# Performance work log

Hardware: AMD Instinct MI355X
Metric: run time of the kernel (lower is better)

## Reference

```python
import jax, jax.numpy as jnp
import numpy as np

N_EXPERTS = 8
TOP_K = 2
D_MODEL = 1024
HIDDEN = 4096


def setup_inputs() -> dict:
    key = jax.random.key(0)
    ks = jax.random.split(key, 6)
    B, S = 4, 1024
    scale = 0.02
    x = jax.random.normal(ks[0], (B, S, D_MODEL), dtype=jnp.float32)
    # gate / noise linear weights, torch nn.Linear convention: (out, in)
    w_gate = jax.random.normal(ks[1], (N_EXPERTS, D_MODEL), dtype=jnp.float32) * scale
    w_noise = jax.random.normal(ks[2], (N_EXPERTS, D_MODEL), dtype=jnp.float32) * scale
    # stacked expert weights: w_g/w_u: (E, H, D), w_d: (E, D, H)
    w_g = jax.random.normal(ks[3], (N_EXPERTS, HIDDEN, D_MODEL), dtype=jnp.float32) * scale
    w_u = jax.random.normal(ks[4], (N_EXPERTS, HIDDEN, D_MODEL), dtype=jnp.float32) * scale
    w_d = jax.random.normal(ks[5], (N_EXPERTS, D_MODEL, HIDDEN), dtype=jnp.float32) * scale
    return {"x": x, "w_gate": w_gate, "w_noise": w_noise, "w_g": w_g, "w_u": w_u, "w_d": w_d}


def reference(x, w_gate, w_noise, w_g, w_u, w_d):
    B, S, D = x.shape
    T = B * S
    xf = x.reshape(T, D)

    # --- NoisyTopKGate (eval mode: no noise) ---
    logits = xf @ w_gate.T                                  # (T, E)
    top_logits, top_idx = jax.lax.top_k(logits, TOP_K)      # (T, K)
    top_gates = jax.nn.softmax(top_logits, axis=-1)         # (T, K)
    rows = jnp.arange(T)[:, None]
    gates = jnp.zeros_like(logits).at[rows, top_idx].set(top_gates)  # (T, E) sparse

    probs = jax.nn.softmax(logits, axis=-1)
    f = gates.mean(axis=0)
    P = probs.mean(axis=0)
    aux_loss = N_EXPERTS * jnp.sum(f * P)

    # --- expert loop (SwiGLU FFN); gate==0 zeroes non-routed contributions ---
    out = jnp.zeros_like(xf)
    for e in range(N_EXPERTS):
        hidden = jax.nn.silu(xf @ w_g[e].T) * (xf @ w_u[e].T)   # (T, H)
        y = hidden @ w_d[e].T                                    # (T, D)
        out = out + gates[:, e:e + 1] * y

    return out.reshape(B, S, D), aux_loss
```

## Files before the change

### kernel.cpp

```cpp
#include <hip/hip_runtime.h>

#define TT 4096
#define DM 1024
#define HH 4096
#define NE 8
#define NSLOT (TT*2)
#define TM 128
#define MAXTILES 72

typedef __bf16 bf16x8 __attribute__((ext_vector_type(8)));
typedef float f32x4 __attribute__((ext_vector_type(4)));

__device__ __forceinline__ unsigned short f2bs(float f) {
  unsigned u = __float_as_uint(f);
  u += 0x7fffu + ((u >> 16) & 1u);
  return (unsigned short)(u >> 16);
}
__device__ __forceinline__ float bs2f(unsigned short s) {
  return __uint_as_float(((unsigned)s) << 16);
}
__device__ __forceinline__ unsigned pk_rnd(float lo, float hi) {
  return ((__float_as_uint(lo) + 0x8000u) >> 16) |
         ((__float_as_uint(hi) + 0x8000u) & 0xffff0000u);
}
__device__ __forceinline__ void gld_lds16(const unsigned short* g, unsigned short* l) {
  __builtin_amdgcn_global_load_lds(
      (const __attribute__((address_space(1))) unsigned int*)g,
      (__attribute__((address_space(3))) unsigned int*)l, 16, 0, 0);
}

__global__ __launch_bounds__(256) void k_gate(
    const float* __restrict__ x, const float* __restrict__ w_gate,
    int* __restrict__ counts, float* __restrict__ gsum, float* __restrict__ psum,
    int* __restrict__ gidx, float* __restrict__ gval) {
  __shared__ float wg[NE * DM];
  __shared__ float bg[NE]; __shared__ float bp[NE]; __shared__ int bc[NE];
  int tid = threadIdx.x;
  for (int i = tid; i < NE * DM; i += 256) wg[i] = w_gate[i];
  if (tid < NE) { bg[tid] = 0.f; bp[tid] = 0.f; bc[tid] = 0; }
  __syncthreads();
  int wave = tid >> 6, lane = tid & 63;
  for (int it = 0; it < 4; ++it) {
    int t = blockIdx.x * 16 + wave * 4 + it;
    const float* xr = x + (size_t)t * DM;
    float s[NE];
#pragma unroll
    for (int e = 0; e < NE; ++e) s[e] = 0.f;
    for (int d = lane; d < DM; d += 64) {
      float xv = xr[d];
#pragma unroll
      for (int e = 0; e < NE; ++e) s[e] += xv * wg[e * DM + d];
    }
#pragma unroll
    for (int e = 0; e < NE; ++e) {
      float v = s[e];
      v += __shfl_down(v, 32); v += __shfl_down(v, 16); v += __shfl_down(v, 8);
      v += __shfl_down(v, 4);  v += __shfl_down(v, 2);  v += __shfl_down(v, 1);
      s[e] = v;
    }
    if (lane == 0) {
      int e1 = 0; float v1 = s[0];
      for (int e = 1; e < NE; ++e) if (s[e] > v1) { v1 = s[e]; e1 = e; }
      int e2 = -1; float v2 = -1e30f;
      for (int e = 0; e < NE; ++e) if (e != e1 && s[e] > v2) { v2 = s[e]; e2 = e; }
      float g1 = 1.f / (1.f + __expf(v2 - v1));
      float g2 = 1.f - g1;
      float psm = 0.f, p[NE];
      for (int e = 0; e < NE; ++e) { p[e] = __expf(s[e] - v1); psm += p[e]; }
      float inv = 1.f / psm;
      atomicAdd(&bg[e1], g1); atomicAdd(&bg[e2], g2);
      for (int e = 0; e < NE; ++e) atomicAdd(&bp[e], p[e] * inv);
      atomicAdd(&bc[e1], 1); atomicAdd(&bc[e2], 1);
      gidx[t * 2] = e1; gidx[t * 2 + 1] = e2;
      gval[t * 2] = g1; gval[t * 2 + 1] = g2;
    }
  }
  __syncthreads();
  if (tid < NE) {
    atomicAdd(&counts[tid], bc[tid]);
    atomicAdd(&gsum[tid], bg[tid]);
    atomicAdd(&psum[tid], bp[tid]);
  }
}

__global__ void k_plan(const int* __restrict__ counts, const float* __restrict__ gsum,
                       const float* __restrict__ psum, int* __restrict__ bases,
                       int* __restrict__ ntiles, int* __restrict__ tile_e,
                       int* __restrict__ tile_s0, int* __restrict__ tile_n,
                       float* __restrict__ aux_out) {
  if (threadIdx.x != 0 || blockIdx.x != 0) return;
  int base = 0, nt = 0;
  for (int e = 0; e < NE; ++e) {
    bases[e] = base;
    int c = counts[e];
    for (int s = 0; s < c; s += TM) {
      tile_e[nt] = e; tile_s0[nt] = base + s;
      tile_n[nt] = (c - s < TM) ? (c - s) : TM; ++nt;
    }
    base += c;
  }
  *ntiles = nt;
  float aux = 0.f;
  for (int e = 0; e < NE; ++e)
    aux += (gsum[e] / (float)TT) * (psum[e] / (float)TT);
  *aux_out = aux * (float)NE;
}

__global__ __launch_bounds__(256) void k_scatter(
    const int* __restrict__ gidx, const int* __restrict__ bases,
    int* __restrict__ cursor, int* __restrict__ stok, int* __restrict__ t2s) {
  int t = blockIdx.x * 256 + threadIdx.x;
#pragma unroll
  for (int k = 0; k < 2; ++k) {
    int e = gidx[t * 2 + k];
    int pos = atomicAdd(&cursor[e], 1);
    int slot = bases[e] + pos;
    stok[slot] = t;
    t2s[t * 2 + k] = slot;
  }
}

__global__ __launch_bounds__(256) void k_gather(
    const float* __restrict__ x, const int* __restrict__ stok,
    unsigned short* __restrict__ abuf) {
  int gid = blockIdx.x * 256 + threadIdx.x;
  int slot = gid >> 7;
  int d0 = (gid & 127) << 3;
  int tok = stok[slot];
  const float* src = x + (size_t)tok * DM + d0;
  float4 v0 = *(const float4*)src;
  float4 v1 = *(const float4*)(src + 4);
  uint4 pk;
  pk.x = pk_rnd(v0.x, v0.y); pk.y = pk_rnd(v0.z, v0.w);
  pk.z = pk_rnd(v1.x, v1.y); pk.w = pk_rnd(v1.z, v1.w);
  *(uint4*)(abuf + (size_t)slot * DM + d0) = pk;
}

__global__ __launch_bounds__(256) void k_ffn1(
    const unsigned short* __restrict__ abuf, const float* __restrict__ w_g,
    const float* __restrict__ w_u, const int* __restrict__ ntiles,
    const int* __restrict__ tile_e, const int* __restrict__ tile_s0,
    const int* __restrict__ tile_n, unsigned short* __restrict__ hbuf) {
  int mt = blockIdx.x;
  if (mt >= *ntiles) return;
  int e = tile_e[mt], s0 = tile_s0[mt], nrows = tile_n[mt];
  int n0 = blockIdx.y * 64;
  __shared__ unsigned short As[TM * 32];
  __shared__ unsigned short Bg[64 * 32];
  __shared__ unsigned short Bu[64 * 32];
  int tid = threadIdx.x, wid = tid >> 6, lane = tid & 63;
  int wm = (wid >> 1) * 64, wn = (wid & 1) * 32;
  int l15 = lane & 15, lq = lane >> 4;

  const unsigned short* ap =
      abuf + (size_t)(s0 + wid * 32 + (lane >> 2)) * DM + (lane & 3) * 8;
  unsigned short* al0 = As + (wid * 32) * 32;
  unsigned short* al1 = As + (wid * 32 + 16) * 32;

  int nb = tid >> 2, k8 = (tid & 3) << 3;
  const float* gp = w_g + ((size_t)e * HH + (size_t)(n0 + nb)) * DM + k8;
  const float* up = w_u + ((size_t)e * HH + (size_t)(n0 + nb)) * DM + k8;
  unsigned short* bgl = Bg + nb * 32 + k8;
  unsigned short* bul = Bu + nb * 32 + k8;

  f32x4 accg[4][2], accu[4][2];
#pragma unroll
  for (int i = 0; i < 4; ++i)
#pragma unroll
    for (int j = 0; j < 2; ++j) {
      accg[i][j] = (f32x4){0.f, 0.f, 0.f, 0.f};
      accu[i][j] = (f32x4){0.f, 0.f, 0.f, 0.f};
    }

  for (int kb = 0; kb < DM; kb += 32) {
    __syncthreads();
    gld_lds16(ap + kb, al0);
    gld_lds16(ap + kb + 16 * DM, al1);
    float4 g0 = *(const float4*)(gp + kb);
    float4 g1 = *(const float4*)(gp + kb + 4);
    float4 u0 = *(const float4*)(up + kb);
    float4 u1 = *(const float4*)(up + kb + 4);
    uint4 pg, pu;
    pg.x = pk_rnd(g0.x, g0.y); pg.y = pk_rnd(g0.z, g0.w);
    pg.z = pk_rnd(g1.x, g1.y); pg.w = pk_rnd(g1.z, g1.w);
    pu.x = pk_rnd(u0.x, u0.y); pu.y = pk_rnd(u0.z, u0.w);
    pu.z = pk_rnd(u1.x, u1.y); pu.w = pk_rnd(u1.z, u1.w);
    *(uint4*)bgl = pg;
    *(uint4*)bul = pu;
    __syncthreads();
    bf16x8 af[4], bgf[2], buf_[2];
#pragma unroll
    for (int mi = 0; mi < 4; ++mi)
      af[mi] = *(const bf16x8*)&As[(wm + mi * 16 + l15) * 32 + lq * 8];
#pragma unroll
    for (int ni = 0; ni < 2; ++ni) {
      bgf[ni] = *(const bf16x8*)&Bg[(wn + ni * 16 + l15) * 32 + lq * 8];
      buf_[ni] = *(const bf16x8*)&Bu[(wn + ni * 16 + l15) * 32 + lq * 8];
    }
#pragma unroll
    for (int mi = 0; mi < 4; ++mi)
#pragma unroll
      for (int ni = 0; ni < 2; ++ni) {
        accg[mi][ni] = __builtin_amdgcn_mfma_f32_16x16x32_bf16(
            af[mi], bgf[ni], accg[mi][ni], 0, 0, 0);
        accu[mi][ni] = __builtin_amdgcn_mfma_f32_16x16x32_bf16(
            af[mi], buf_[ni], accu[mi][ni], 0, 0, 0);
      }
  }

#pragma unroll
  for (int mi = 0; mi < 4; ++mi)
#pragma unroll
    for (int r = 0; r < 4; ++r) {
      int m_loc = wm + mi * 16 + lq * 4 + r;
      if (m_loc < nrows) {
#pragma unroll
        for (int ni = 0; ni < 2; ++ni) {
          float g = accg[mi][ni][r], u = accu[mi][ni][r];
          float h = g / (1.f + __expf(-g)) * u;
          int n = n0 + wn + ni * 16 + l15;
          hbuf[(size_t)(s0 + m_loc) * HH + n] = f2bs(h);
        }
      }
    }
}

__global__ __launch_bounds__(256) void k_ffn2(
    const unsigned short* __restrict__ hbuf, const float* __restrict__ w_d,
    const int* __restrict__ ntiles, const int* __restrict__ tile_e,
    const int* __restrict__ tile_s0, const int* __restrict__ tile_n,
    unsigned short* __restrict__ ybuf) {
  int mt = blockIdx.x;
  if (mt >= *ntiles) return;
  int e = tile_e[mt], s0 = tile_s0[mt], nrows = tile_n[mt];
  int n0 = blockIdx.y * 64;
  __shared__ unsigned short As[TM * 32];
  __shared__ unsigned short Bs[64 * 32];
  int tid = threadIdx.x, wid = tid >> 6, lane = tid & 63;
  int wm = (wid >> 1) * 64, wn = (wid & 1) * 32;
  int l15 = lane & 15, lq = lane >> 4;

  const unsigned short* ap =
      hbuf + (size_t)(s0 + wid * 32 + (lane >> 2)) * HH + (lane & 3) * 8;
  unsigned short* al0 = As + (wid * 32) * 32;
  unsigned short* al1 = As + (wid * 32 + 16) * 32;

  int nb = tid >> 2, k8 = (tid & 3) << 3;
  const float* dp = w_d + ((size_t)e * DM + (size_t)(n0 + nb)) * HH + k8;
  unsigned short* bl = Bs + nb * 32 + k8;

  f32x4 acc[4][2];
#pragma unroll
  for (int i = 0; i < 4; ++i)
#pragma unroll
    for (int j = 0; j < 2; ++j) acc[i][j] = (f32x4){0.f, 0.f, 0.f, 0.f};

  for (int kb = 0; kb < HH; kb += 32) {
    __syncthreads();
    gld_lds16(ap + kb, al0);
    gld_lds16(ap + kb + 16 * HH, al1);
    float4 d0 = *(const float4*)(dp + kb);
    float4 d1 = *(const float4*)(dp + kb + 4);
    uint4 pd;
    pd.x = pk_rnd(d0.x, d0.y); pd.y = pk_rnd(d0.z, d0.w);
    pd.z = pk_rnd(d1.x, d1.y); pd.w = pk_rnd(d1.z, d1.w);
    *(uint4*)bl = pd;
    __syncthreads();
    bf16x8 af[4], bf[2];
#pragma unroll
    for (int mi = 0; mi < 4; ++mi)
      af[mi] = *(const bf16x8*)&As[(wm + mi * 16 + l15) * 32 + lq * 8];
#pragma unroll
    for (int ni = 0; ni < 2; ++ni)
      bf[ni] = *(const bf16x8*)&Bs[(wn + ni * 16 + l15) * 32 + lq * 8];
#pragma unroll
    for (int mi = 0; mi < 4; ++mi)
#pragma unroll
      for (int ni = 0; ni < 2; ++ni)
        acc[mi][ni] = __builtin_amdgcn_mfma_f32_16x16x32_bf16(
            af[mi], bf[ni], acc[mi][ni], 0, 0, 0);
  }

#pragma unroll
  for (int mi = 0; mi < 4; ++mi)
#pragma unroll
    for (int r = 0; r < 4; ++r) {
      int m_loc = wm + mi * 16 + lq * 4 + r;
      if (m_loc < nrows) {
#pragma unroll
        for (int ni = 0; ni < 2; ++ni) {
          int n = n0 + wn + ni * 16 + l15;
          ybuf[(size_t)(s0 + m_loc) * DM + n] = f2bs(acc[mi][ni][r]);
        }
      }
    }
}

__global__ __launch_bounds__(256) void k_combine(
    const unsigned short* __restrict__ ybuf, const int* __restrict__ t2s,
    const float* __restrict__ gval, float* __restrict__ out) {
  int gid = blockIdx.x * 256 + threadIdx.x;
  int t = gid >> 8;
  int d0 = (gid & 255) << 2;
  int s1 = t2s[t * 2], s2 = t2s[t * 2 + 1];
  float g1 = gval[t * 2], g2 = gval[t * 2 + 1];
  ushort4 y1 = *(const ushort4*)(ybuf + (size_t)s1 * DM + d0);
  ushort4 y2 = *(const ushort4*)(ybuf + (size_t)s2 * DM + d0);
  float4 o;
  o.x = g1 * bs2f(y1.x) + g2 * bs2f(y2.x);
  o.y = g1 * bs2f(y1.y) + g2 * bs2f(y2.y);
  o.z = g1 * bs2f(y1.z) + g2 * bs2f(y2.z);
  o.w = g1 * bs2f(y1.w) + g2 * bs2f(y2.w);
  *(float4*)(out + (size_t)t * DM + d0) = o;
}

extern "C" void kernel_launch(void* const* d_in, const int* in_sizes, int n_in,
                              void* d_out, int out_size, void* d_ws, size_t ws_size,
                              hipStream_t stream) {
  const float* x      = (const float*)d_in[0];
  const float* w_gate = (const float*)d_in[1];
  const float* w_g    = (const float*)d_in[3];
  const float* w_u    = (const float*)d_in[4];
  const float* w_d    = (const float*)d_in[5];
  float* out = (float*)d_out;

  char* ws = (char*)d_ws;
  int*   counts  = (int*)(ws + 0);
  int*   cursor  = (int*)(ws + 32);
  float* gsum    = (float*)(ws + 64);
  float* psum    = (float*)(ws + 96);
  int*   ntiles  = (int*)(ws + 128);
  int*   bases   = (int*)(ws + 192);
  int*   tile_e  = (int*)(ws + 4096);
  int*   tile_s0 = (int*)(ws + 4608);
  int*   tile_n  = (int*)(ws + 5120);
  int*   gidx    = (int*)(ws + 16384);
  float* gval    = (float*)(ws + 49152);
  int*   stok    = (int*)(ws + 81920);
  int*   t2s     = (int*)(ws + 114688);
  unsigned short* abuf = (unsigned short*)(ws + (1 << 20));
  unsigned short* ybuf = abuf;
  unsigned short* hbuf = (unsigned short*)(ws + 18874368);

  hipMemsetAsync(ws, 0, 256, stream);
  k_gate<<<256, 256, 0, stream>>>(x, w_gate, counts, gsum, psum, gidx, gval);
  k_plan<<<1, 64, 0, stream>>>(counts, gsum, psum, bases, ntiles, tile_e, tile_s0,
                               tile_n, out + (size_t)TT * DM);
  k_scatter<<<TT / 256, 256, 0, stream>>>(gidx, bases, cursor, stok, t2s);
  k_gather<<<NSLOT * 128 / 256, 256, 0, stream>>>(x, stok, abuf);
  k_ffn1<<<dim3(MAXTILES, HH / 64), 256, 0, stream>>>(abuf, w_g, w_u, ntiles,
                                                      tile_e, tile_s0, tile_n, hbuf);
  k_ffn2<<<dim3(MAXTILES, DM / 64), 256, 0, stream>>>(hbuf, w_d, ntiles, tile_e,
                                                      tile_s0, tile_n, ybuf);
  k_combine<<<(TT * DM / 4) / 256, 256, 0, stream>>>(ybuf, t2s, gval, out);
}
```

Before: 938.6 us.

## Pre-convert expert weights to bf16 once per call and load via direct LDS

Adds a kernel that converts all w_g, w_u and w_d weights to bf16 in workspace each call. The FFN kernels then load the weights straight into LDS with the same async global-to-LDS path used for activations, instead of converting fp32 in registers inside every tile. Without this, every tile re-reads and re-converts the fp32 weights. ffn2 also widens its N tile to 128 to reuse the A tile more. The cost is an extra pass over all weights (read 384MB fp32, write 192MB bf16), and the new path only runs if the workspace is large enough.

```diff
diff --git a/kernel.cpp b/kernel.cpp
--- a/kernel.cpp
+++ b/kernel.cpp
@@ -136,7 +136,170 @@
   *(uint4*)(abuf + (size_t)slot * DM + d0) = pk;
 }
 
-__global__ __launch_bounds__(256) void k_ffn1(
+__global__ __launch_bounds__(256) void k_wconv3(
+    const float* __restrict__ a, const float* __restrict__ b, const float* __restrict__ c,
+    unsigned short* __restrict__ da, unsigned short* __restrict__ db,
+    unsigned short* __restrict__ dc) {
+  int gid = blockIdx.x * 256 + threadIdx.x;
+  int seg = gid >> 22;
+  size_t idx = (size_t)(gid & 0x3fffff) * 8;
+  const float* s = (seg == 0 ? a : seg == 1 ? b : c) + idx;
+  unsigned short* d = (seg == 0 ? da : seg == 1 ? db : dc) + idx;
+  float4 v0 = *(const float4*)s;
+  float4 v1 = *(const float4*)(s + 4);
+  uint4 pk;
+  pk.x = pk_rnd(v0.x, v0.y); pk.y = pk_rnd(v0.z, v0.w);
+  pk.z = pk_rnd(v1.x, v1.y); pk.w = pk_rnd(v1.z, v1.w);
+  *(uint4*)d = pk;
+}
+
+
+__global__ __launch_bounds__(256) void k_ffn1_bf(
+    const unsigned short* __restrict__ abuf, const unsigned short* __restrict__ wgb,
+    const unsigned short* __restrict__ wub, const int* __restrict__ ntiles,
+    const int* __restrict__ tile_e, const int* __restrict__ tile_s0,
+    const int* __restrict__ tile_n, unsigned short* __restrict__ hbuf) {
+  int mt = blockIdx.x;
+  if (mt >= *ntiles) return;
+  int e = tile_e[mt], s0 = tile_s0[mt], nrows = tile_n[mt];
+  int n0 = blockIdx.y * 64;
+  __shared__ unsigned short As[TM * 32];
+  __shared__ unsigned short Bg[64 * 32];
+  __shared__ unsigned short Bu[64 * 32];
+  int tid = threadIdx.x, wid = tid >> 6, lane = tid & 63;
+  int wm = (wid >> 1) * 64, wn = (wid & 1) * 32;
+  int l15 = lane & 15, lq = lane >> 4;
+  int lrow = lane >> 2, lcol = (lane & 3) << 3;
+
+  const unsigned short* ap = abuf + (size_t)(s0 + wid * 32 + lrow) * DM + lcol;
+  unsigned short* al0 = As + (wid * 32) * 32;
+  unsigned short* al1 = As + (wid * 32 + 16) * 32;
+  const unsigned short* bgp = wgb + ((size_t)e * HH + (size_t)(n0 + wid * 16 + lrow)) * DM + lcol;
+  const unsigned short* bup = wub + ((size_t)e * HH + (size_t)(n0 + wid * 16 + lrow)) * DM + lcol;
+  unsigned short* bgl = Bg + (wid * 16) * 32;
+  unsigned short* bul = Bu + (wid * 16) * 32;
+
+  f32x4 accg[4][2], accu[4][2];
+#pragma unroll
+  for (int i = 0; i < 4; ++i)
+#pragma unroll
+    for (int j = 0; j < 2; ++j) {
+      accg[i][j] = (f32x4){0.f, 0.f, 0.f, 0.f};
+      accu[i][j] = (f32x4){0.f, 0.f, 0.f, 0.f};
+    }
+
+  for (int kb = 0; kb < DM; kb += 32) {
+    __syncthreads();
+    gld_lds16(ap + kb, al0);
+    gld_lds16(ap + kb + 16 * DM, al1);
+    gld_lds16(bgp + kb, bgl);
+    gld_lds16(bup + kb, bul);
+    __syncthreads();
+    bf16x8 af[4], bgf[2], buf_[2];
+#pragma unroll
+    for (int mi = 0; mi < 4; ++mi)
+      af[mi] = *(const bf16x8*)&As[(wm + mi * 16 + l15) * 32 + lq * 8];
+#pragma unroll
+    for (int ni = 0; ni < 2; ++ni) {
+      bgf[ni] = *(const bf16x8*)&Bg[(wn + ni * 16 + l15) * 32 + lq * 8];
+      buf_[ni] = *(const bf16x8*)&Bu[(wn + ni * 16 + l15) * 32 + lq * 8];
+    }
+#pragma unroll
+    for (int mi = 0; mi < 4; ++mi)
+#pragma unroll
+      for (int ni = 0; ni < 2; ++ni) {
+        accg[mi][ni] = __builtin_amdgcn_mfma_f32_16x16x32_bf16(
+            af[mi], bgf[ni], accg[mi][ni], 0, 0, 0);
+        accu[mi][ni] = __builtin_amdgcn_mfma_f32_16x16x32_bf16(
+            af[mi], buf_[ni], accu[mi][ni], 0, 0, 0);
+      }
+  }
+
+#pragma unroll
+  for (int mi = 0; mi < 4; ++mi)
+#pragma unroll
+    for (int r = 0; r < 4; ++r) {
+      int m_loc = wm + mi * 16 + lq * 4 + r;
+      if (m_loc < nrows) {
+#pragma unroll
+        for (int ni = 0; ni < 2; ++ni) {
+          float g = accg[mi][ni][r], u = accu[mi][ni][r];
+          float h = g / (1.f + __expf(-g)) * u;
+          int n = n0 + wn + ni * 16 + l15;
+          hbuf[(size_t)(s0 + m_loc) * HH + n] = f2bs(h);
+        }
+      }
+    }
+}
+
+__global__ __launch_bounds__(256) void k_ffn2_bf(
+    const unsigned short* __restrict__ hbuf, const unsigned short* __restrict__ wdb,
+    const int* __restrict__ ntiles, const int* __restrict__ tile_e,
+    const int* __restrict__ tile_s0, const int* __restrict__ tile_n,
+    unsigned short* __restrict__ ybuf) {
+  int mt = blockIdx.x;
+  if (mt >= *ntiles) return;
+  int e = tile_e[mt], s0 = tile_s0[mt], nrows = tile_n[mt];
+  int n0 = blockIdx.y * 128;
+  __shared__ unsigned short As[TM * 32];
+  __shared__ unsigned short Bs[128 * 32];
+  int tid = threadIdx.x, wid = tid >> 6, lane = tid & 63;
+  int wm = (wid >> 1) * 64, wn = (wid & 1) * 64;
+  int l15 = lane & 15, lq = lane >> 4;
+  int lrow = lane >> 2, lcol = (lane & 3) << 3;
+
+  const unsigned short* ap = hbuf + (size_t)(s0 + wid * 32 + lrow) * HH + lcol;
+  unsigned short* al0 = As + (wid * 32) * 32;
+  unsigned short* al1 = As + (wid * 32 + 16) * 32;
+  const unsigned short* bp = wdb + ((size_t)e * DM + (size_t)(n0 + wid * 32 + lrow)) * HH + lcol;
+  unsigned short* bl0 = Bs + (wid * 32) * 32;
+  unsigned short* bl1 = Bs + (wid * 32 + 16) * 32;
+
+  f32x4 acc[4][4];
+#pragma unroll
+  for (int i = 0; i < 4; ++i)
+#pragma unroll
+    for (int j = 0; j < 4; ++j) acc[i][j] = (f32x4){0.f, 0.f, 0.f, 0.f};
+
+  for (int kb = 0; kb < HH; kb += 32) {
+    __syncthreads();
+    gld_lds16(ap + kb, al0);
+    gld_lds16(ap + kb + 16 * HH, al1);
+    gld_lds16(bp + kb, bl0);
+    gld_lds16(bp + kb + 16 * HH, bl1);
+    __syncthreads();
+    bf16x8 af[4], bf[4];
+#pragma unroll
+    for (int mi = 0; mi < 4; ++mi)
+      af[mi] = *(const bf16x8*)&As[(wm + mi * 16 + l15) * 32 + lq * 8];
+#pragma unroll
+    for (int ni = 0; ni < 4; ++ni)
+      bf[ni] = *(const bf16x8*)&Bs[(wn + ni * 16 + l15) * 32 + lq * 8];
+#pragma unroll
+    for (int mi = 0; mi < 4; ++mi)
+#pragma unroll
+      for (int ni = 0; ni < 4; ++ni)
+        acc[mi][ni] = __builtin_amdgcn_mfma_f32_16x16x32_bf16(
+            af[mi], bf[ni], acc[mi][ni], 0, 0, 0);
+  }
+
+#pragma unroll
+  for (int mi = 0; mi < 4; ++mi)
+#pragma unroll
+    for (int r = 0; r < 4; ++r) {
+      int m_loc = wm + mi * 16 + lq * 4 + r;
+      if (m_loc < nrows) {
+#pragma unroll
+        for (int ni = 0; ni < 4; ++ni) {
+          int n = n0 + wn + ni * 16 + l15;
+          ybuf[(size_t)(s0 + m_loc) * DM + n] = f2bs(acc[mi][ni][r]);
+        }
+      }
+    }
+}
+
+
+__global__ __launch_bounds__(256) void k_ffn1_f32(
     const unsigned short* __restrict__ abuf, const float* __restrict__ w_g,
     const float* __restrict__ w_u, const int* __restrict__ ntiles,
     const int* __restrict__ tile_e, const int* __restrict__ tile_s0,
@@ -151,18 +314,15 @@
   int tid = threadIdx.x, wid = tid >> 6, lane = tid & 63;
   int wm = (wid >> 1) * 64, wn = (wid & 1) * 32;
   int l15 = lane & 15, lq = lane >> 4;
-
   const unsigned short* ap =
       abuf + (size_t)(s0 + wid * 32 + (lane >> 2)) * DM + (lane & 3) * 8;
   unsigned short* al0 = As + (wid * 32) * 32;
   unsigned short* al1 = As + (wid * 32 + 16) * 32;
-
   int nb = tid >> 2, k8 = (tid & 3) << 3;
   const float* gp = w_g + ((size_t)e * HH + (size_t)(n0 + nb)) * DM + k8;
   const float* up = w_u + ((size_t)e * HH + (size_t)(n0 + nb)) * DM + k8;
   unsigned short* bgl = Bg + nb * 32 + k8;
   unsigned short* bul = Bu + nb * 32 + k8;
-
   f32x4 accg[4][2], accu[4][2];
 #pragma unroll
   for (int i = 0; i < 4; ++i)
@@ -171,7 +331,6 @@
       accg[i][j] = (f32x4){0.f, 0.f, 0.f, 0.f};
       accu[i][j] = (f32x4){0.f, 0.f, 0.f, 0.f};
     }
-
   for (int kb = 0; kb < DM; kb += 32) {
     __syncthreads();
     gld_lds16(ap + kb, al0);
@@ -207,7 +366,6 @@
             af[mi], buf_[ni], accu[mi][ni], 0, 0, 0);
       }
   }
-
 #pragma unroll
   for (int mi = 0; mi < 4; ++mi)
 #pragma unroll
@@ -225,7 +383,7 @@
     }
 }
 
-__global__ __launch_bounds__(256) void k_ffn2(
+__global__ __launch_bounds__(256) void k_ffn2_f32(
     const unsigned short* __restrict__ hbuf, const float* __restrict__ w_d,
     const int* __restrict__ ntiles, const int* __restrict__ tile_e,
     const int* __restrict__ tile_s0, const int* __restrict__ tile_n,
@@ -239,22 +397,18 @@
   int tid = threadIdx.x, wid = tid >> 6, lane = tid & 63;
   int wm = (wid >> 1) * 64, wn = (wid & 1) * 32;
   int l15 = lane & 15, lq = lane >> 4;
-
   const unsigned short* ap =
       hbuf + (size_t)(s0 + wid * 32 + (lane >> 2)) * HH + (lane & 3) * 8;
   unsigned short* al0 = As + (wid * 32) * 32;
   unsigned short* al1 = As + (wid * 32 + 16) * 32;
-
   int nb = tid >> 2, k8 = (tid & 3) << 3;
   const float* dp = w_d + ((size_t)e * DM + (size_t)(n0 + nb)) * HH + k8;
   unsigned short* bl = Bs + nb * 32 + k8;
-
   f32x4 acc[4][2];
 #pragma unroll
   for (int i = 0; i < 4; ++i)
 #pragma unroll
     for (int j = 0; j < 2; ++j) acc[i][j] = (f32x4){0.f, 0.f, 0.f, 0.f};
-
   for (int kb = 0; kb < HH; kb += 32) {
     __syncthreads();
     gld_lds16(ap + kb, al0);
@@ -280,7 +434,6 @@
         acc[mi][ni] = __builtin_amdgcn_mfma_f32_16x16x32_bf16(
             af[mi], bf[ni], acc[mi][ni], 0, 0, 0);
   }
-
 #pragma unroll
   for (int mi = 0; mi < 4; ++mi)
 #pragma unroll
@@ -338,9 +491,13 @@
   float* gval    = (float*)(ws + 49152);
   int*   stok    = (int*)(ws + 81920);
   int*   t2s     = (int*)(ws + 114688);
-  unsigned short* abuf = (unsigned short*)(ws + (1 << 20));
+  unsigned short* abuf = (unsigned short*)(ws + (1ull << 20));
   unsigned short* ybuf = abuf;
-  unsigned short* hbuf = (unsigned short*)(ws + 18874368);
+  unsigned short* hbuf = (unsigned short*)(ws + (18ull << 20));
+  unsigned short* wgb = (unsigned short*)(ws + (84ull << 20));
+  unsigned short* wub = (unsigned short*)(ws + (148ull << 20));
+  unsigned short* wdb = (unsigned short*)(ws + (212ull << 20));
+  const bool pre = ws_size >= (277ull << 20);
 
   hipMemsetAsync(ws, 0, 256, stream);
   k_gate<<<256, 256, 0, stream>>>(x, w_gate, counts, gsum, psum, gidx, gval);
@@ -348,9 +505,17 @@
                                tile_n, out + (size_t)TT * DM);
   k_scatter<<<TT / 256, 256, 0, stream>>>(gidx, bases, cursor, stok, t2s);
   k_gather<<<NSLOT * 128 / 256, 256, 0, stream>>>(x, stok, abuf);
-  k_ffn1<<<dim3(MAXTILES, HH / 64), 256, 0, stream>>>(abuf, w_g, w_u, ntiles,
-                                                      tile_e, tile_s0, tile_n, hbuf);
-  k_ffn2<<<dim3(MAXTILES, DM / 64), 256, 0, stream>>>(hbuf, w_d, ntiles, tile_e,
-                                                      tile_s0, tile_n, ybuf);
+  if (pre) {
+    k_wconv3<<<3 * (NE * HH * DM / 8) / 256, 256, 0, stream>>>(w_g, w_u, w_d, wgb, wub, wdb);
+    k_ffn1_bf<<<dim3(MAXTILES, HH / 64), 256, 0, stream>>>(abuf, wgb, wub, ntiles,
+                                                           tile_e, tile_s0, tile_n, hbuf);
+    k_ffn2_bf<<<dim3(MAXTILES, DM / 128), 256, 0, stream>>>(hbuf, wdb, ntiles, tile_e,
+                                                            tile_s0, tile_n, ybuf);
+  } else {
+    k_ffn1_f32<<<dim3(MAXTILES, HH / 64), 256, 0, stream>>>(abuf, w_g, w_u, ntiles,
+                                                            tile_e, tile_s0, tile_n, hbuf);
+    k_ffn2_f32<<<dim3(MAXTILES, DM / 64), 256, 0, stream>>>(hbuf, w_d, ntiles, tile_e,
+                                                            tile_s0, tile_n, ybuf);
+  }
   k_combine<<<(TT * DM / 4) / 256, 256, 0, stream>>>(ybuf, t2s, gval, out);
 }
```

Result: faster. 833.5 us (-11.2%).
